# Optimization experiments

Measured on AMD Instinct MI355X. Metric: run time of the kernel, lower is better.

## Reference

```python
import jax, jax.numpy as jnp
import numpy as np

D_MODEL = 1024
N_HEADS = 16
B, T = 2, 2048


def setup_inputs() -> dict:
    key = jax.random.key(0)
    ks = jax.random.split(key, 6)
    scale = D_MODEL ** -0.5
    # additive causal mask: 0 on/below diagonal, large negative above
    neg = jnp.float32(-1e9)
    causal = jnp.where(jnp.tril(jnp.ones((T, T), dtype=bool)), 0.0, neg)
    mask = causal[None, None, :, :].astype(jnp.float32)  # [1,1,T,T]
    return {
        'x': jax.random.normal(ks[0], (B, T, D_MODEL), dtype=jnp.float32),
        'mask': mask,
        'Wq': jax.random.normal(ks[1], (D_MODEL, D_MODEL), dtype=jnp.float32) * scale,
        'bq': jnp.zeros((D_MODEL,), jnp.float32),
        'Wk': jax.random.normal(ks[2], (D_MODEL, D_MODEL), dtype=jnp.float32) * scale,
        'bk': jnp.zeros((D_MODEL,), jnp.float32),
        'Wv': jax.random.normal(ks[3], (D_MODEL, D_MODEL), dtype=jnp.float32) * scale,
        'bv': jnp.zeros((D_MODEL,), jnp.float32),
        'Wo': jax.random.normal(ks[4], (D_MODEL, D_MODEL), dtype=jnp.float32) * scale,
        'bo': jnp.zeros((D_MODEL,), jnp.float32),
    }


def reference(x, mask, Wq, bq, Wk, bk, Wv, bv, Wo, bo):
    B_, T_, D_ = x.shape
    H = N_HEADS
    hd = D_ // H
    q = (x @ Wq + bq).reshape(B_, T_, H, hd)
    k = (x @ Wk + bk).reshape(B_, T_, H, hd)
    v = (x @ Wv + bv).reshape(B_, T_, H, hd)
    # full BxHxTxT scores (faithful to non-flash original)
    attn = jnp.einsum('bthd,bshd->bhts', q, k) * (hd ** -0.5)
    attn = attn + mask
    attn = jax.nn.softmax(attn, axis=-1)
    out = jnp.einsum('bhts,bshd->bthd', attn, v).reshape(B_, T_, D_)
    return out @ Wo + bo
```

## Files before the change

kernel.cpp:

```cpp
#include <hip/hip_runtime.h>
#include <hip/hip_bf16.h>
#include <math.h>

#define D_MODEL 1024
#define N_HEADS 16
#define HD 64
#define BB 2
#define TT 2048
#define MROWS (BB*TT)

typedef __attribute__((ext_vector_type(8))) short short8;
typedef __attribute__((ext_vector_type(4))) float f32x4;

static __device__ __forceinline__ void gload16(const void* g, void* l) {
    __builtin_amdgcn_global_load_lds(
        (const __attribute__((address_space(1))) void*)g,
        (__attribute__((address_space(3))) void*)l, 16, 0, 0);
}

static __device__ __forceinline__ unsigned short f2bf(float f) {
    union { float f; unsigned u; } x; x.f = f;
    unsigned r = (x.u + 0x7fffu + ((x.u >> 16) & 1u)) >> 16;
    return (unsigned short)r;
}

static __device__ __forceinline__ unsigned pack_bf16x2(float lo, float hi) {
    union { float f; unsigned u; } a, b; a.f = lo; b.f = hi;
    return __builtin_amdgcn_perm(b.u + 0x8000u, a.u + 0x8000u, 0x07060302u);
}

__global__ __launch_bounds__(256) void cast_x_kernel(
    const float* __restrict__ x, unsigned short* __restrict__ xb)
{
    int i = (blockIdx.x * 256 + threadIdx.x) * 8;
    float4 a = *(const float4*)(x + i);
    float4 b = *(const float4*)(x + i + 4);
    short8 o;
    o[0] = f2bf(a.x); o[1] = f2bf(a.y); o[2] = f2bf(a.z); o[3] = f2bf(a.w);
    o[4] = f2bf(b.x); o[5] = f2bf(b.y); o[6] = f2bf(b.z); o[7] = f2bf(b.w);
    *(short8*)(xb + i) = o;
}

__global__ __launch_bounds__(256) void pack_w4_kernel(
    const float* __restrict__ Wq, const float* __restrict__ Wk,
    const float* __restrict__ Wv, const float* __restrict__ Wo,
    unsigned short* __restrict__ Wqkvt, unsigned short* __restrict__ Wot)
{
    __shared__ float Ts[64][65];
    const int z = blockIdx.z;
    const float* W = (z == 0) ? Wq : (z == 1) ? Wk : (z == 2) ? Wv : Wo;
    unsigned short* Wt = (z < 3) ? (Wqkvt + (size_t)z * 1024 * 1024) : Wot;
    const int tid = threadIdx.x;
    const int n0 = blockIdx.x * 64, k0 = blockIdx.y * 64;
#pragma unroll
    for (int i = 0; i < 16; ++i) {
        int lin = i * 256 + tid;
        int kl = lin >> 6, nl = lin & 63;
        Ts[nl][kl] = W[(size_t)(k0 + kl) * 1024 + n0 + nl];
    }
    __syncthreads();
#pragma unroll
    for (int i = 0; i < 16; ++i) {
        int lin = i * 256 + tid;
        int nl = lin >> 6, kl = lin & 63;
        Wt[(size_t)(n0 + nl) * 1024 + k0 + kl] = f2bf(Ts[nl][kl]);
    }
}

__global__ void pack_bias_kernel(const float* __restrict__ bq,
                                 const float* __restrict__ bk,
                                 const float* __restrict__ bv,
                                 float* __restrict__ bqkv)
{
    int i = blockIdx.x * 256 + threadIdx.x;
    float v = (i < 1024) ? bq[i] : ((i < 2048) ? bk[i - 1024] : bv[i - 2048]);
    bqkv[i] = v;
}

__global__ __launch_bounds__(256) void vtrans_kernel(
    const unsigned short* __restrict__ QKV, unsigned short* __restrict__ Vt)
{
    __shared__ unsigned short Ts[64][65];
    const int tid = threadIdx.x;
    const int bx = blockIdx.x;
    const int st = bx & 31, h = (bx >> 5) & 15, b = bx >> 9;
    const int s0 = st * 64;
#pragma unroll
    for (int i = 0; i < 16; ++i) {
        int lin = i * 256 + tid;
        int sl = lin >> 6, dl = lin & 63;
        Ts[dl][sl] = QKV[(size_t)(b * TT + s0 + sl) * 3072 + 2048 + h * 64 + dl];
    }
    __syncthreads();
#pragma unroll
    for (int i = 0; i < 16; ++i) {
        int lin = i * 256 + tid;
        int dl = lin >> 6, sl = lin & 63;
        Vt[(size_t)((b * 16 + h) * 64 + dl) * TT + s0 + sl] = Ts[dl][sl];
    }
}

__global__ __launch_bounds__(256) void gemm_mfma_kernel(
    const unsigned short* __restrict__ A, const unsigned short* __restrict__ Bt,
    const float* __restrict__ bias, void* __restrict__ Cout,
    int N, int K, int bf16out, int qcols)
{
    __shared__ __align__(16) unsigned short As[128 * 32];
    __shared__ __align__(16) unsigned short Bs[128 * 32];

    const int tid  = threadIdx.x;
    const int lane = tid & 63;
    const int ln   = lane & 15;
    const int qd   = lane >> 4;
    const int w    = tid >> 6;
    const int wm   = w >> 1, wn = w & 1;
    const int row0 = blockIdx.y * 128;
    const int col0 = blockIdx.x * 128;

    f32x4 acc[4][4];
#pragma unroll
    for (int mi = 0; mi < 4; ++mi)
#pragma unroll
        for (int ni = 0; ni < 4; ++ni)
            acc[mi][ni] = (f32x4){0.f, 0.f, 0.f, 0.f};

    const int s0 = tid, s1 = tid + 256;
    const int rA0 = s0 >> 2, cA0 = (s0 & 3) ^ ((rA0 >> 1) & 3);
    const int rA1 = s1 >> 2, cA1 = (s1 & 3) ^ ((rA1 >> 1) & 3);
    const unsigned short* Ag0 = A + (size_t)(row0 + rA0) * K + cA0 * 8;
    const unsigned short* Ag1 = A + (size_t)(row0 + rA1) * K + cA1 * 8;
    const unsigned short* Bg0 = Bt + (size_t)(col0 + rA0) * K + cA0 * 8;
    const unsigned short* Bg1 = Bt + (size_t)(col0 + rA1) * K + cA1 * 8;
    unsigned short* AsL0 = As + s0 * 8;
    unsigned short* AsL1 = As + s1 * 8;
    unsigned short* BsL0 = Bs + s0 * 8;
    unsigned short* BsL1 = Bs + s1 * 8;

    for (int kb = 0; kb < K; kb += 32) {
        if (kb) __syncthreads();
        gload16(Ag0 + kb, AsL0);
        gload16(Ag1 + kb, AsL1);
        gload16(Bg0 + kb, BsL0);
        gload16(Bg1 + kb, BsL1);
        __builtin_amdgcn_s_waitcnt(0);
        __syncthreads();

        short8 af[4], bf[4];
#pragma unroll
        for (int i = 0; i < 4; ++i) {
            int ra = wm * 64 + i * 16 + ln;
            int pa = ra * 4 + (qd ^ ((ra >> 1) & 3));
            af[i] = *(const short8*)(As + pa * 8);
            int rb = wn * 64 + i * 16 + ln;
            int pb = rb * 4 + (qd ^ ((rb >> 1) & 3));
            bf[i] = *(const short8*)(Bs + pb * 8);
        }
#pragma unroll
        for (int mi = 0; mi < 4; ++mi)
#pragma unroll
            for (int ni = 0; ni < 4; ++ni)
                acc[mi][ni] = __builtin_amdgcn_mfma_f32_16x16x32_bf16(
                    af[mi], bf[ni], acc[mi][ni], 0, 0, 0);
    }

    float bv[4], scl[4];
#pragma unroll
    for (int ni = 0; ni < 4; ++ni) {
        bv[ni]  = bias[col0 + wn * 64 + ni * 16 + ln];
        scl[ni] = (col0 + wn * 64 + ni * 16 < qcols) ? 0.125f : 1.0f;
    }

#pragma unroll
    for (int mi = 0; mi < 4; ++mi)
#pragma unroll
        for (int ni = 0; ni < 4; ++ni)
#pragma unroll
            for (int r = 0; r < 4; ++r) {
                float v = (acc[mi][ni][r] + bv[ni]) * scl[ni];
                int row = row0 + wm * 64 + mi * 16 + qd * 4 + r;
                int col = col0 + wn * 64 + ni * 16 + ln;
                if (bf16out)
                    ((unsigned short*)Cout)[(size_t)row * N + col] = f2bf(v);
                else
                    ((float*)Cout)[(size_t)row * N + col] = v;
            }
}

#define PSTRIDE 136
#define LDS_TOTAL (4*64*PSTRIDE + 2048)

__global__ __launch_bounds__(256, 2) void attn_mfma_kernel(
    const unsigned short* __restrict__ QKV,
    const unsigned short* __restrict__ Vt,
    unsigned short* __restrict__ Aout)
{
    __shared__ __align__(16) unsigned char lds[LDS_TOTAL];

    const int tid  = threadIdx.x;
    const int lane = tid & 63;
    const int ln   = lane & 15;
    const int qd   = lane >> 4;
    const int qd4  = qd * 4;
    const int w    = tid >> 6;

    const int bx = blockIdx.x;
    const int p  = bx & 15;
    const int h  = (bx >> 4) & 15;
    const int b  = bx >> 8;

    unsigned char* Pb   = lds + w * (64 * PSTRIDE);
    float*         Oacc = (float*)lds;
    float*         mlm  = (float*)(lds + 4 * 64 * PSTRIDE);
    float*         mll  = mlm + 256;

    const unsigned short* Kh = QKV + 1024 + h * 64;
    const unsigned short* Qh = QKV + h * 64;
    const unsigned short* Vh = Vt + (size_t)((b * 16 + h) * 64) * TT;

    for (int ti = 0; ti < 2; ++ti) {
        const int qt = ti ? p : (31 - p);
        __syncthreads();

        short8 qa[4][2];
        {
            const unsigned short* Qb = Qh + (size_t)(b * TT + qt * 64) * 3072;
#pragma unroll
            for (int q4 = 0; q4 < 4; ++q4)
#pragma unroll
                for (int kk = 0; kk < 2; ++kk)
                    qa[q4][kk] = *(const short8*)(Qb + (size_t)(q4 * 16 + ln) * 3072 + kk * 32 + qd * 8);
        }

        f32x4 O[4][4];
#pragma unroll
        for (int dt = 0; dt < 4; ++dt)
#pragma unroll
            for (int q4 = 0; q4 < 4; ++q4)
                O[dt][q4] = (f32x4){0.f, 0.f, 0.f, 0.f};
        float m_i[4] = {-1e30f, -1e30f, -1e30f, -1e30f};
        float l_i[4] = {0.f, 0.f, 0.f, 0.f};

        for (int kc = w; kc <= qt; kc += 4) {
            const unsigned short* Kc = Kh + (size_t)(b * TT + kc * 64) * 3072;
            const unsigned short* Vc = Vh + kc * 64;

            short8 kf[4][2], vf[4][2];
#pragma unroll
            for (int kt = 0; kt < 4; ++kt)
#pragma unroll
                for (int kk = 0; kk < 2; ++kk)
                    kf[kt][kk] = *(const short8*)(Kc + (size_t)(kt * 16 + ln) * 3072 + kk * 32 + qd * 8);
#pragma unroll
            for (int dt = 0; dt < 4; ++dt)
#pragma unroll
                for (int kk = 0; kk < 2; ++kk)
                    vf[dt][kk] = *(const short8*)(Vc + (size_t)(dt * 16 + ln) * TT + kk * 32 + qd * 8);

            f32x4 st[4][4];
#pragma unroll
            for (int kt = 0; kt < 4; ++kt)
#pragma unroll
                for (int q4 = 0; q4 < 4; ++q4) {
                    f32x4 a = (f32x4){0.f, 0.f, 0.f, 0.f};
                    a = __builtin_amdgcn_mfma_f32_16x16x32_bf16(kf[kt][0], qa[q4][0], a, 0, 0, 0);
                    a = __builtin_amdgcn_mfma_f32_16x16x32_bf16(kf[kt][1], qa[q4][1], a, 0, 0, 0);
                    st[kt][q4] = a;
                }

            if (kc == qt) {
#pragma unroll
                for (int kt = 0; kt < 4; ++kt)
#pragma unroll
                    for (int q4 = 0; q4 < 4; ++q4)
#pragma unroll
                        for (int r = 0; r < 4; ++r)
                            if (kt * 16 + qd4 + r > q4 * 16 + ln)
                                st[kt][q4][r] = -1e30f;
            }

            float alpha[4];
#pragma unroll
            for (int q4 = 0; q4 < 4; ++q4) {
                float mx = st[0][q4][0];
#pragma unroll
                for (int kt = 0; kt < 4; ++kt)
#pragma unroll
                    for (int r = 0; r < 4; ++r)
                        mx = fmaxf(mx, st[kt][q4][r]);
                mx = fmaxf(mx, __shfl_xor(mx, 16, 64));
                mx = fmaxf(mx, __shfl_xor(mx, 32, 64));
                float mn = fmaxf(m_i[q4], mx);
                alpha[q4] = __expf(m_i[q4] - mn);
                m_i[q4] = mn;
            }
#pragma unroll
            for (int kt = 0; kt < 4; ++kt)
#pragma unroll
                for (int q4 = 0; q4 < 4; ++q4)
#pragma unroll
                    for (int r = 0; r < 4; ++r)
                        st[kt][q4][r] = __expf(st[kt][q4][r] - m_i[q4]);
#pragma unroll
            for (int q4 = 0; q4 < 4; ++q4) {
                float sm = 0.f;
#pragma unroll
                for (int kt = 0; kt < 4; ++kt)
#pragma unroll
                    for (int r = 0; r < 4; ++r)
                        sm += st[kt][q4][r];
                sm += __shfl_xor(sm, 16, 64);
                sm += __shfl_xor(sm, 32, 64);
                l_i[q4] = l_i[q4] * alpha[q4] + sm;
            }
#pragma unroll
            for (int dt = 0; dt < 4; ++dt)
#pragma unroll
                for (int q4 = 0; q4 < 4; ++q4) {
                    O[dt][q4][0] *= alpha[q4]; O[dt][q4][1] *= alpha[q4];
                    O[dt][q4][2] *= alpha[q4]; O[dt][q4][3] *= alpha[q4];
                }

#pragma unroll
            for (int kt = 0; kt < 4; ++kt)
#pragma unroll
                for (int q4 = 0; q4 < 4; ++q4) {
                    unsigned u0 = pack_bf16x2(st[kt][q4][0], st[kt][q4][1]);
                    unsigned u1 = pack_bf16x2(st[kt][q4][2], st[kt][q4][3]);
                    *(uint2*)(Pb + (q4 * 16 + ln) * PSTRIDE + kt * 32 + qd * 8) =
                        make_uint2(u0, u1);
                }

#pragma unroll
            for (int kk = 0; kk < 2; ++kk)
#pragma unroll
                for (int q4 = 0; q4 < 4; ++q4) {
                    union { struct { uint2 a, b; } u; short8 s; } y;
                    const unsigned char* yp = Pb + (q4 * 16 + ln) * PSTRIDE + kk * 64 + qd * 16;
                    y.u.a = *(const uint2*)(yp);
                    y.u.b = *(const uint2*)(yp + 8);
#pragma unroll
                    for (int dt = 0; dt < 4; ++dt)
                        O[dt][q4] = __builtin_amdgcn_mfma_f32_16x16x32_bf16(
                            vf[dt][kk], y.s, O[dt][q4], 0, 0, 0);
                }
        }

        if (qd == 0) {
#pragma unroll
            for (int q4 = 0; q4 < 4; ++q4) {
                mlm[w * 64 + q4 * 16 + ln] = m_i[q4];
                mll[w * 64 + q4 * 16 + ln] = l_i[q4];
            }
        }
        __syncthreads();

        float fac[4];
#pragma unroll
        for (int q4 = 0; q4 < 4; ++q4) {
            int q = q4 * 16 + ln;
            float m0 = mlm[q], m1 = mlm[64 + q], m2 = mlm[128 + q], m3 = mlm[192 + q];
            float M = fmaxf(fmaxf(m0, m1), fmaxf(m2, m3));
            float f0 = __expf(m0 - M), f1 = __expf(m1 - M);
            float f2 = __expf(m2 - M), f3 = __expf(m3 - M);
            float L = f0 * mll[q] + f1 * mll[64 + q] + f2 * mll[128 + q] + f3 * mll[192 + q];
            float myf = (w == 0) ? f0 : (w == 1) ? f1 : (w == 2) ? f2 : f3;
            fac[q4] = myf / L;
        }
#pragma unroll
        for (int dt = 0; dt < 4; ++dt)
#pragma unroll
            for (int q4 = 0; q4 < 4; ++q4) {
                O[dt][q4][0] *= fac[q4]; O[dt][q4][1] *= fac[q4];
                O[dt][q4][2] *= fac[q4]; O[dt][q4][3] *= fac[q4];
            }

        for (int wv = 0; wv < 4; ++wv) {
            if (w == wv) {
#pragma unroll
                for (int dt = 0; dt < 4; ++dt)
#pragma unroll
                    for (int q4 = 0; q4 < 4; ++q4) {
                        float* pp = Oacc + (q4 * 16 + ln) * 68 + dt * 16 + qd4;
                        if (wv == 0) {
                            *(f32x4*)pp = O[dt][q4];
                        } else {
                            f32x4 t = *(const f32x4*)pp;
                            t += O[dt][q4];
                            *(f32x4*)pp = t;
                        }
                    }
            }
            __syncthreads();
        }

        {
            int q = tid >> 2, dg = tid & 3;
            const float* rowp = Oacc + q * 68 + dg * 16;
            short8 s0v, s1v;
#pragma unroll
            for (int i = 0; i < 8; ++i) {
                s0v[i] = f2bf(rowp[i]);
                s1v[i] = f2bf(rowp[8 + i]);
            }
            size_t orow = (size_t)(b * TT + qt * 64 + q) * D_MODEL + h * 64 + dg * 16;
            *(short8*)(Aout + orow) = s0v;
            *(short8*)(Aout + orow + 8) = s1v;
        }
    }
}

extern "C" void kernel_launch(void* const* d_in, const int* in_sizes, int n_in,
                              void* d_out, int out_size, void* d_ws, size_t ws_size,
                              hipStream_t stream) {
    const float* x  = (const float*)d_in[0];
    const float* Wq = (const float*)d_in[2];
    const float* bq = (const float*)d_in[3];
    const float* Wk = (const float*)d_in[4];
    const float* bk = (const float*)d_in[5];
    const float* Wv = (const float*)d_in[6];
    const float* bv = (const float*)d_in[7];
    const float* Wo = (const float*)d_in[8];
    const float* bo = (const float*)d_in[9];
    float* out = (float*)d_out;

    uint8_t* w8 = (uint8_t*)d_ws;
    const size_t MB = 1024 * 1024;
    unsigned short* xb    = (unsigned short*)(w8);
    unsigned short* Wqkvt = (unsigned short*)(w8 + 8 * MB);
    unsigned short* Wot   = (unsigned short*)(w8 + 14 * MB);
    float*          bqkv  = (float*)(w8 + 16 * MB);
    unsigned short* QKV   = (unsigned short*)(w8 + 17 * MB);
    unsigned short* Vt    = (unsigned short*)(w8 + 41 * MB);
    unsigned short* Aout  = (unsigned short*)(w8 + 49 * MB);

    cast_x_kernel<<<MROWS * D_MODEL / (256 * 8), 256, 0, stream>>>(x, xb);
    pack_w4_kernel<<<dim3(16, 16, 4), 256, 0, stream>>>(Wq, Wk, Wv, Wo, Wqkvt, Wot);
    pack_bias_kernel<<<12, 256, 0, stream>>>(bq, bk, bv, bqkv);

    gemm_mfma_kernel<<<dim3(24, 32), 256, 0, stream>>>(xb, Wqkvt, bqkv, QKV, 3072, 1024, 1, 1024);
    vtrans_kernel<<<BB * N_HEADS * 32, 256, 0, stream>>>(QKV, Vt);
    attn_mfma_kernel<<<BB * N_HEADS * 16, 256, 0, stream>>>(QKV, Vt, Aout);
    gemm_mfma_kernel<<<dim3(8, 32), 256, 0, stream>>>(Aout, Wot, bo, out, 1024, 1024, 0, 0);
}
```

Before: 215.2 us.

## Merge prep kernels, fuse V transpose into QKV GEMM, XCD-swizzle GEMM tiles

Folds the x cast, the weight packing and the bias packing into one prep kernel, which removes two launches. The QKV GEMM epilogue now writes V straight into the transposed Vt layout, so the separate vtrans pass and its read and write of V are gone. Both GEMMs remap block indices so that neighbouring tiles land on the same XCD, aiming for better L2 reuse. The output projection uses a new 128x64 tile kernel that doubles the block count for better occupancy. The Vt stores are strided 8-byte writes, which may coalesce less well than the old transpose kernel did.

```diff
diff --git a/kernel.cpp b/kernel.cpp
--- a/kernel.cpp
+++ b/kernel.cpp
@@ -29,81 +29,57 @@
     return __builtin_amdgcn_perm(b.u + 0x8000u, a.u + 0x8000u, 0x07060302u);
 }
 
-__global__ __launch_bounds__(256) void cast_x_kernel(
-    const float* __restrict__ x, unsigned short* __restrict__ xb)
-{
-    int i = (blockIdx.x * 256 + threadIdx.x) * 8;
-    float4 a = *(const float4*)(x + i);
-    float4 b = *(const float4*)(x + i + 4);
-    short8 o;
-    o[0] = f2bf(a.x); o[1] = f2bf(a.y); o[2] = f2bf(a.z); o[3] = f2bf(a.w);
-    o[4] = f2bf(b.x); o[5] = f2bf(b.y); o[6] = f2bf(b.z); o[7] = f2bf(b.w);
-    *(short8*)(xb + i) = o;
-}
-
-__global__ __launch_bounds__(256) void pack_w4_kernel(
+__global__ __launch_bounds__(256) void prep_kernel(
+    const float* __restrict__ x,
     const float* __restrict__ Wq, const float* __restrict__ Wk,
     const float* __restrict__ Wv, const float* __restrict__ Wo,
-    unsigned short* __restrict__ Wqkvt, unsigned short* __restrict__ Wot)
+    const float* __restrict__ bq, const float* __restrict__ bk,
+    const float* __restrict__ bv,
+    unsigned short* __restrict__ xb, unsigned short* __restrict__ Wqkvt,
+    unsigned short* __restrict__ Wot, float* __restrict__ bqkv)
 {
     __shared__ float Ts[64][65];
-    const int z = blockIdx.z;
-    const float* W = (z == 0) ? Wq : (z == 1) ? Wk : (z == 2) ? Wv : Wo;
-    unsigned short* Wt = (z < 3) ? (Wqkvt + (size_t)z * 1024 * 1024) : Wot;
-    const int tid = threadIdx.x;
-    const int n0 = blockIdx.x * 64, k0 = blockIdx.y * 64;
-#pragma unroll
-    for (int i = 0; i < 16; ++i) {
-        int lin = i * 256 + tid;
-        int kl = lin >> 6, nl = lin & 63;
-        Ts[nl][kl] = W[(size_t)(k0 + kl) * 1024 + n0 + nl];
-    }
-    __syncthreads();
-#pragma unroll
-    for (int i = 0; i < 16; ++i) {
-        int lin = i * 256 + tid;
-        int nl = lin >> 6, kl = lin & 63;
-        Wt[(size_t)(n0 + nl) * 1024 + k0 + kl] = f2bf(Ts[nl][kl]);
-    }
-}
-
-__global__ void pack_bias_kernel(const float* __restrict__ bq,
-                                 const float* __restrict__ bk,
-                                 const float* __restrict__ bv,
-                                 float* __restrict__ bqkv)
-{
-    int i = blockIdx.x * 256 + threadIdx.x;
-    float v = (i < 1024) ? bq[i] : ((i < 2048) ? bk[i - 1024] : bv[i - 2048]);
-    bqkv[i] = v;
-}
-
-__global__ __launch_bounds__(256) void vtrans_kernel(
-    const unsigned short* __restrict__ QKV, unsigned short* __restrict__ Vt)
-{
-    __shared__ unsigned short Ts[64][65];
-    const int tid = threadIdx.x;
-    const int bx = blockIdx.x;
-    const int st = bx & 31, h = (bx >> 5) & 15, b = bx >> 9;
-    const int s0 = st * 64;
-#pragma unroll
-    for (int i = 0; i < 16; ++i) {
-        int lin = i * 256 + tid;
-        int sl = lin >> 6, dl = lin & 63;
-        Ts[dl][sl] = QKV[(size_t)(b * TT + s0 + sl) * 3072 + 2048 + h * 64 + dl];
-    }
-    __syncthreads();
-#pragma unroll
-    for (int i = 0; i < 16; ++i) {
-        int lin = i * 256 + tid;
-        int dl = lin >> 6, sl = lin & 63;
-        Vt[(size_t)((b * 16 + h) * 64 + dl) * TT + s0 + sl] = Ts[dl][sl];
+    const int bx = blockIdx.x, tid = threadIdx.x;
+    if (bx < 1024) {
+        const int z = bx >> 8, rem = bx & 255;
+        const float* W = (z == 0) ? Wq : (z == 1) ? Wk : (z == 2) ? Wv : Wo;
+        unsigned short* Wt = (z < 3) ? (Wqkvt + (size_t)z * 1024 * 1024) : Wot;
+        const int n0 = (rem & 15) * 64, k0 = (rem >> 4) * 64;
+#pragma unroll
+        for (int i = 0; i < 16; ++i) {
+            int lin = i * 256 + tid;
+            int kl = lin >> 6, nl = lin & 63;
+            Ts[nl][kl] = W[(size_t)(k0 + kl) * 1024 + n0 + nl];
+        }
+        __syncthreads();
+#pragma unroll
+        for (int i = 0; i < 16; ++i) {
+            int lin = i * 256 + tid;
+            int nl = lin >> 6, kl = lin & 63;
+            Wt[(size_t)(n0 + nl) * 1024 + k0 + kl] = f2bf(Ts[nl][kl]);
+        }
+    } else if (bx < 3072) {
+        int i = ((bx - 1024) * 256 + tid) * 8;
+        float4 a = *(const float4*)(x + i);
+        float4 b = *(const float4*)(x + i + 4);
+        short8 o;
+        o[0] = f2bf(a.x); o[1] = f2bf(a.y); o[2] = f2bf(a.z); o[3] = f2bf(a.w);
+        o[4] = f2bf(b.x); o[5] = f2bf(b.y); o[6] = f2bf(b.z); o[7] = f2bf(b.w);
+        *(short8*)(xb + i) = o;
+    } else {
+#pragma unroll
+        for (int j = 0; j < 12; ++j) {
+            int i = j * 256 + tid;
+            float v = (i < 1024) ? bq[i] : ((i < 2048) ? bk[i - 1024] : bv[i - 2048]);
+            bqkv[i] = v;
+        }
     }
 }
 
 __global__ __launch_bounds__(256) void gemm_mfma_kernel(
     const unsigned short* __restrict__ A, const unsigned short* __restrict__ Bt,
-    const float* __restrict__ bias, void* __restrict__ Cout,
-    int N, int K, int bf16out, int qcols)
+    const float* __restrict__ bias, unsigned short* __restrict__ Cout,
+    unsigned short* __restrict__ Vt, int N, int K, int qcols)
 {
     __shared__ __align__(16) unsigned short As[128 * 32];
     __shared__ __align__(16) unsigned short Bs[128 * 32];
@@ -114,8 +90,15 @@
     const int qd   = lane >> 4;
     const int w    = tid >> 6;
     const int wm   = w >> 1, wn = w & 1;
-    const int row0 = blockIdx.y * 128;
-    const int col0 = blockIdx.x * 128;
+
+    const int lin  = blockIdx.y * gridDim.x + blockIdx.x;
+    const int xcd  = lin & 7;
+    const int slot = lin >> 3;
+    const int sxw  = gridDim.x >> 1;
+    const int syw  = ((gridDim.x * gridDim.y) >> 3) / sxw;
+    const int sx   = slot % sxw, sy = slot / sxw;
+    const int row0 = ((xcd >> 1) * syw + sy) * 128;
+    const int col0 = ((xcd & 1) * sxw + sx) * 128;
 
     f32x4 acc[4][4];
 #pragma unroll
@@ -163,26 +146,131 @@
                     af[mi], bf[ni], acc[mi][ni], 0, 0, 0);
     }
 
-    float bv[4], scl[4];
-#pragma unroll
-    for (int ni = 0; ni < 4; ++ni) {
-        bv[ni]  = bias[col0 + wn * 64 + ni * 16 + ln];
-        scl[ni] = (col0 + wn * 64 + ni * 16 < qcols) ? 0.125f : 1.0f;
+    float bv[4];
+#pragma unroll
+    for (int ni = 0; ni < 4; ++ni)
+        bv[ni] = bias[col0 + wn * 64 + ni * 16 + ln];
+
+    if (col0 >= 2048) {
+        const int h = ((col0 - 2048) >> 6) + wn;
+#pragma unroll
+        for (int mi = 0; mi < 4; ++mi) {
+            int row = row0 + wm * 64 + mi * 16 + qd * 4;
+            int b = row >> 11, t = row & 2047;
+#pragma unroll
+            for (int ni = 0; ni < 4; ++ni) {
+                int d = ni * 16 + ln;
+                float v0 = acc[mi][ni][0] + bv[ni];
+                float v1 = acc[mi][ni][1] + bv[ni];
+                float v2 = acc[mi][ni][2] + bv[ni];
+                float v3 = acc[mi][ni][3] + bv[ni];
+                unsigned u0 = pack_bf16x2(v0, v1);
+                unsigned u1 = pack_bf16x2(v2, v3);
+                *(uint2*)(Vt + (size_t)((b * 16 + h) * 64 + d) * TT + t) =
+                    make_uint2(u0, u1);
+            }
+        }
+    } else {
+        float scl[4];
+#pragma unroll
+        for (int ni = 0; ni < 4; ++ni)
+            scl[ni] = (col0 + wn * 64 + ni * 16 < qcols) ? 0.125f : 1.0f;
+#pragma unroll
+        for (int mi = 0; mi < 4; ++mi)
+#pragma unroll
+            for (int ni = 0; ni < 4; ++ni)
+#pragma unroll
+                for (int r = 0; r < 4; ++r) {
+                    float v = (acc[mi][ni][r] + bv[ni]) * scl[ni];
+                    int row = row0 + wm * 64 + mi * 16 + qd * 4 + r;
+                    int col = col0 + wn * 64 + ni * 16 + ln;
+                    Cout[(size_t)row * N + col] = f2bf(v);
+                }
     }
-
-#pragma unroll
-    for (int mi = 0; mi < 4; ++mi)
+}
+
+__global__ __launch_bounds__(256) void gemm_mfma_n64_kernel(
+    const unsigned short* __restrict__ A, const unsigned short* __restrict__ Bt,
+    const float* __restrict__ bias, float* __restrict__ Cout, int N, int K)
+{
+    __shared__ __align__(16) unsigned short As[128 * 32];
+    __shared__ __align__(16) unsigned short Bs[64 * 32];
+
+    const int tid  = threadIdx.x;
+    const int lane = tid & 63;
+    const int ln   = lane & 15;
+    const int qd   = lane >> 4;
+    const int w    = tid >> 6;
+
+    const int lin  = blockIdx.y * gridDim.x + blockIdx.x;
+    const int xcd  = lin & 7;
+    const int slot = lin >> 3;
+    const int sxw  = gridDim.x >> 1;
+    const int syw  = ((gridDim.x * gridDim.y) >> 3) / sxw;
+    const int sx   = slot % sxw, sy = slot / sxw;
+    const int row0 = ((xcd >> 1) * syw + sy) * 128;
+    const int col0 = ((xcd & 1) * sxw + sx) * 64;
+
+    f32x4 acc[2][4];
+#pragma unroll
+    for (int mi = 0; mi < 2; ++mi)
 #pragma unroll
         for (int ni = 0; ni < 4; ++ni)
+            acc[mi][ni] = (f32x4){0.f, 0.f, 0.f, 0.f};
+
+    const int s0 = tid, s1 = tid + 256;
+    const int rA0 = s0 >> 2, cA0 = (s0 & 3) ^ ((rA0 >> 1) & 3);
+    const int rA1 = s1 >> 2, cA1 = (s1 & 3) ^ ((rA1 >> 1) & 3);
+    const unsigned short* Ag0 = A + (size_t)(row0 + rA0) * K + cA0 * 8;
+    const unsigned short* Ag1 = A + (size_t)(row0 + rA1) * K + cA1 * 8;
+    const unsigned short* Bg0 = Bt + (size_t)(col0 + rA0) * K + cA0 * 8;
+    unsigned short* AsL0 = As + s0 * 8;
+    unsigned short* AsL1 = As + s1 * 8;
+    unsigned short* BsL0 = Bs + s0 * 8;
+
+    for (int kb = 0; kb < K; kb += 32) {
+        if (kb) __syncthreads();
+        gload16(Ag0 + kb, AsL0);
+        gload16(Ag1 + kb, AsL1);
+        gload16(Bg0 + kb, BsL0);
+        __builtin_amdgcn_s_waitcnt(0);
+        __syncthreads();
+
+        short8 af[2], bf[4];
+#pragma unroll
+        for (int i = 0; i < 2; ++i) {
+            int ra = w * 32 + i * 16 + ln;
+            int pa = ra * 4 + (qd ^ ((ra >> 1) & 3));
+            af[i] = *(const short8*)(As + pa * 8);
+        }
+#pragma unroll
+        for (int i = 0; i < 4; ++i) {
+            int rb = i * 16 + ln;
+            int pb = rb * 4 + (qd ^ ((rb >> 1) & 3));
+            bf[i] = *(const short8*)(Bs + pb * 8);
+        }
+#pragma unroll
+        for (int mi = 0; mi < 2; ++mi)
+#pragma unroll
+            for (int ni = 0; ni < 4; ++ni)
+                acc[mi][ni] = __builtin_amdgcn_mfma_f32_16x16x32_bf16(
+                    af[mi], bf[ni], acc[mi][ni], 0, 0, 0);
+    }
+
+    float bv[4];
+#pragma unroll
+    for (int ni = 0; ni < 4; ++ni)
+        bv[ni] = bias[col0 + ni * 16 + ln];
+
+#pragma unroll
+    for (int mi = 0; mi < 2; ++mi)
+#pragma unroll
+        for (int ni = 0; ni < 4; ++ni)
 #pragma unroll
             for (int r = 0; r < 4; ++r) {
-                float v = (acc[mi][ni][r] + bv[ni]) * scl[ni];
-                int row = row0 + wm * 64 + mi * 16 + qd * 4 + r;
-                int col = col0 + wn * 64 + ni * 16 + ln;
-                if (bf16out)
-                    ((unsigned short*)Cout)[(size_t)row * N + col] = f2bf(v);
-                else
-                    ((float*)Cout)[(size_t)row * N + col] = v;
+                int row = row0 + w * 32 + mi * 16 + qd * 4 + r;
+                int col = col0 + ni * 16 + ln;
+                Cout[(size_t)row * N + col] = acc[mi][ni][r] + bv[ni];
             }
 }
 
@@ -433,12 +521,11 @@
     unsigned short* Vt    = (unsigned short*)(w8 + 41 * MB);
     unsigned short* Aout  = (unsigned short*)(w8 + 49 * MB);
 
-    cast_x_kernel<<<MROWS * D_MODEL / (256 * 8), 256, 0, stream>>>(x, xb);
-    pack_w4_kernel<<<dim3(16, 16, 4), 256, 0, stream>>>(Wq, Wk, Wv, Wo, Wqkvt, Wot);
-    pack_bias_kernel<<<12, 256, 0, stream>>>(bq, bk, bv, bqkv);
-
-    gemm_mfma_kernel<<<dim3(24, 32), 256, 0, stream>>>(xb, Wqkvt, bqkv, QKV, 3072, 1024, 1, 1024);
-    vtrans_kernel<<<BB * N_HEADS * 32, 256, 0, stream>>>(QKV, Vt);
+    prep_kernel<<<3073, 256, 0, stream>>>(x, Wq, Wk, Wv, Wo, bq, bk, bv,
+                                          xb, Wqkvt, Wot, bqkv);
+    gemm_mfma_kernel<<<dim3(24, 32), 256, 0, stream>>>(xb, Wqkvt, bqkv, QKV, Vt,
+                                                       3072, 1024, 1024);
     attn_mfma_kernel<<<BB * N_HEADS * 16, 256, 0, stream>>>(QKV, Vt, Aout);
-    gemm_mfma_kernel<<<dim3(8, 32), 256, 0, stream>>>(Aout, Wot, bo, out, 1024, 1024, 0, 0);
-}
+    gemm_mfma_n64_kernel<<<dim3(16, 32), 256, 0, stream>>>(Aout, Wot, bo, out,
+                                                           1024, 1024);
+}
```

After: 197.8 us. 1.09x faster.
